# Optimization experiments

Measured on AMD Instinct MI355X. Metric: run time of the kernel, lower is better.

## Reference

```python
import jax, jax.numpy as jnp
import numpy as np

PS = 16
E = 512          # embed_dim
H = 8            # num_heads
EPS = 1e-5


def _ln(x, g, b):
    m = jnp.mean(x, axis=-1, keepdims=True)
    v = jnp.mean((x - m) ** 2, axis=-1, keepdims=True)
    return (x - m) * jax.lax.rsqrt(v + EPS) * g + b


def _mha(q_in, kv_in, in_w, in_b, out_w, out_b):
    # torch nn.MultiheadAttention: packed in_proj [3E, E], out_proj [E, E]
    Bq, Lq, _ = q_in.shape
    Lk = kv_in.shape[1]
    d = E // H
    wq, wk, wv = jnp.split(in_w, 3, axis=0)
    bq, bk, bv = jnp.split(in_b, 3, axis=0)
    q = (q_in @ wq.T + bq).reshape(Bq, Lq, H, d)
    k = (kv_in @ wk.T + bk).reshape(Bq, Lk, H, d)
    v = (kv_in @ wv.T + bv).reshape(Bq, Lk, H, d)
    scores = jnp.einsum('bqhd,bkhd->bhqk', q, k) / jnp.sqrt(jnp.float32(d))
    a = jax.nn.softmax(scores, axis=-1)
    o = jnp.einsum('bhqk,bkhd->bqhd', a, v).reshape(Bq, Lq, E)
    return o @ out_w.T + out_b


def setup_inputs() -> dict:
    key = jax.random.key(0)
    ks = jax.random.split(key, 24)
    s = 0.02
    D = 3 * PS * PS
    inp = {
        'neighbor_patches': jax.random.normal(ks[0], (8, 32, 32, 9, 3, PS, PS), jnp.float32),
        'w_pe': jax.random.normal(ks[1], (E, D), jnp.float32) * s,
        'b_pe': jnp.zeros((E,), jnp.float32),
        'pos_embed': jax.random.normal(ks[2], (1, 9, E), jnp.float32),
        'sa_in_w': jax.random.normal(ks[3], (3 * E, E), jnp.float32) * s,
        'sa_in_b': jnp.zeros((3 * E,), jnp.float32),
        'sa_out_w': jax.random.normal(ks[4], (E, E), jnp.float32) * s,
        'sa_out_b': jnp.zeros((E,), jnp.float32),
        'g1': jnp.ones((E,), jnp.float32), 'beta1': jnp.zeros((E,), jnp.float32),
        'ca_in_w': jax.random.normal(ks[5], (3 * E, E), jnp.float32) * s,
        'ca_in_b': jnp.zeros((3 * E,), jnp.float32),
        'ca_out_w': jax.random.normal(ks[6], (E, E), jnp.float32) * s,
        'ca_out_b': jnp.zeros((E,), jnp.float32),
        'g2': jnp.ones((E,), jnp.float32), 'beta2': jnp.zeros((E,), jnp.float32),
        'w1': jax.random.normal(ks[7], (4 * E, E), jnp.float32) * s,
        'b1': jnp.zeros((4 * E,), jnp.float32),
        'w2': jax.random.normal(ks[8], (E, 4 * E), jnp.float32) * s,
        'b2': jnp.zeros((E,), jnp.float32),
        'g3': jnp.ones((E,), jnp.float32), 'beta3': jnp.zeros((E,), jnp.float32),
    }
    return inp


def reference(neighbor_patches, w_pe, b_pe, pos_embed,
              sa_in_w, sa_in_b, sa_out_w, sa_out_b, g1, beta1,
              ca_in_w, ca_in_b, ca_out_w, ca_out_b, g2, beta2,
              w1, b1, w2, b2, g3, beta3):
    B, NH, NW, NN, C, ps, _ = neighbor_patches.shape
    x = neighbor_patches.reshape(B * NH * NW, NN, C * ps * ps)
    x = x @ w_pe.T + b_pe                       # [BN, 9, E]
    x = x + pos_embed
    attn = _mha(x, x, sa_in_w, sa_in_b, sa_out_w, sa_out_b)
    x = _ln(x + attn, g1, beta1)
    cq = x[:, 4:5, :]                            # center query [BN, 1, E]
    attn = _mha(cq, x, ca_in_w, ca_in_b, ca_out_w, ca_out_b)
    c = _ln(cq + attn, g2, beta2)
    ffn = jax.nn.gelu(c @ w1.T + b1, approximate=False) @ w2.T + b2
    out = _ln(c + ffn, g3, beta3)
    return out[:, 0, :].reshape(B, NH * NW, E)
```

## Files before the change

### kernel.cpp

```cpp
#include <hip/hip_runtime.h>


typedef unsigned short u16;
typedef u16   u16x8 __attribute__((ext_vector_type(8)));
typedef u16   u16x4 __attribute__((ext_vector_type(4)));
typedef __bf16 bf16x8 __attribute__((ext_vector_type(8)));
typedef __bf16 bf16x4 __attribute__((ext_vector_type(4)));
typedef float f32x4 __attribute__((ext_vector_type(4)));

static __device__ __forceinline__ u16 f2bf(float f) {
  union { float f; unsigned u; } v; v.f = f;
  unsigned r = v.u + 0x7FFFu + ((v.u >> 16) & 1u);
  return (u16)(r >> 16);
}
static __device__ __forceinline__ float bf2f(u16 u) {
  union { unsigned u; float f; } v; v.u = ((unsigned)u) << 16;
  return v.f;
}

static __device__ __forceinline__ void gld16(const void* g, void* l) {
  __builtin_amdgcn_global_load_lds(
      (__attribute__((address_space(1))) unsigned int*)(size_t)g,
      (__attribute__((address_space(3))) unsigned int*)(unsigned)(size_t)l,
      16, 0, 0);
}

static __device__ __forceinline__ int xcd_swz(int bid, int nwg) {
  int q = nwg >> 3, r = nwg & 7;
  int xcd = bid & 7, sub = bid >> 3;
  return (xcd < r ? xcd * (q + 1) : r * (q + 1) + (xcd - r) * q) + sub;
}

#define BAR   __builtin_amdgcn_s_barrier()
#define VM0   asm volatile("s_waitcnt vmcnt(0)" ::: "memory")
#define VM2   asm volatile("s_waitcnt vmcnt(2)" ::: "memory")
#define LGKM0 asm volatile("s_waitcnt lgkmcnt(0)" ::: "memory")

template<bool A_F32, bool HAS_POS, bool HAS_RES, bool HAS_GELU>
__global__ __launch_bounds__(256, 4) void gemm_k2(
    const void* Av, int lda,
    const u16* __restrict__ W,
    const float* __restrict__ bias,
    const float* __restrict__ pos,
    const u16* res, int res_stride,
    u16* out,
    int M, int N, int K, int nbx)
{
  __shared__ u16 As[2][4096];
  __shared__ u16 Bs[2][4096];

  const int t    = threadIdx.x;
  const int lane = t & 63, wv = t >> 6;
  const int swz  = xcd_swz(blockIdx.x, gridDim.x);
  const int bm   = (swz / nbx) * 128, bn = (swz % nbx) * 128;
  const int wr   = wv >> 1, wc = wv & 1;

  const int srow = lane >> 2;
  const int skk  = (((lane & 3) ^ ((lane >> 3) & 3)) << 3);
  const int lr = lane & 15;
  const int rg = (((lane >> 4) ^ ((lr >> 1) & 3)) << 3);

  f32x4 acc[4][4] = {};
  float4 areg[4];

  auto stage = [&](int buf, int kt) {
    const u16* A = (const u16*)Av;
    #pragma unroll
    for (int c = 0; c < 2; ++c) {
      int rr = (wv + 4 * c) * 16 + srow;
      gld16(A + (size_t)(bm + rr) * lda + kt * 32 + skk, &As[buf][(wv + 4 * c) * 512]);
      gld16(W + (size_t)(bn + rr) * K   + kt * 32 + skk, &Bs[buf][(wv + 4 * c) * 512]);
    }
  };
  auto stageB = [&](int buf, int kt) {
    #pragma unroll
    for (int c = 0; c < 2; ++c) {
      int rr = (wv + 4 * c) * 16 + srow;
      gld16(W + (size_t)(bn + rr) * K + kt * 32 + skk, &Bs[buf][(wv + 4 * c) * 512]);
    }
  };
  auto loadAf32 = [&](int kt) {
    const float* A = (const float*)Av;
    #pragma unroll
    for (int i = 0; i < 4; ++i) {
      int idx = i * 256 + t, r = idx >> 3, c4 = (idx & 7) * 4;
      areg[i] = *(const float4*)(A + (size_t)(bm + r) * lda + kt * 32 + c4);
    }
  };
  auto writeAf32 = [&](int buf) {
    #pragma unroll
    for (int i = 0; i < 4; ++i) {
      int idx = i * 256 + t, r = idx >> 3, c4 = (idx & 7) * 4;
      int g = (c4 >> 3) ^ ((r >> 1) & 3);
      int off = r * 32 + g * 8 + (c4 & 4);
      bf16x4 h;
      h.x = (__bf16)areg[i].x; h.y = (__bf16)areg[i].y;
      h.z = (__bf16)areg[i].z; h.w = (__bf16)areg[i].w;
      *(u16x4*)&As[buf][off] = *(u16x4*)&h;
    }
  };

  const int nkt = K >> 5;
  if constexpr (A_F32) {
    loadAf32(0); stageB(0, 0);
    VM2;  writeAf32(0);
    VM0; LGKM0; BAR;
  } else {
    stage(0, 0);
    VM0; BAR;
  }

  int cur = 0;
  for (int kt = 0; kt < nkt; ++kt) {
    const bool pf = (kt + 1 < nkt);
    if (pf) {
      if constexpr (A_F32) { loadAf32(kt + 1); stageB(cur ^ 1, kt + 1); }
      else                 { stage(cur ^ 1, kt + 1); }
    }

    bf16x8 a[4], b[4];
    #pragma unroll
    for (int m = 0; m < 4; ++m)
      a[m] = *(const bf16x8*)&As[cur][(wr * 64 + m * 16 + lr) * 32 + rg];
    #pragma unroll
    for (int n = 0; n < 4; ++n)
      b[n] = *(const bf16x8*)&Bs[cur][(wc * 64 + n * 16 + lr) * 32 + rg];
    #pragma unroll
    for (int m = 0; m < 4; ++m)
      #pragma unroll
      for (int n = 0; n < 4; ++n)
        acc[m][n] = __builtin_amdgcn_mfma_f32_16x16x32_bf16(a[m], b[n], acc[m][n], 0, 0, 0);

    if (pf) {
      if constexpr (A_F32) { VM2; writeAf32(cur ^ 1); VM0; LGKM0; }
      else                 { VM0; }
    }
    BAR;
    cur ^= 1;
  }

  const int lq = lane >> 4;
  #pragma unroll
  for (int m = 0; m < 4; ++m) {
    #pragma unroll
    for (int n = 0; n < 4; ++n) {
      int col = bn + wc * 64 + n * 16 + lr;
      float bv = bias[col];
      #pragma unroll
      for (int r = 0; r < 4; ++r) {
        int row = bm + wr * 64 + m * 16 + lq * 4 + r;
        float v = acc[m][n][r] + bv;
        if constexpr (HAS_POS) v += pos[(row % 9) * 512 + col];
        if constexpr (HAS_RES) v += bf2f(res[(size_t)row * res_stride + col]);
        if constexpr (HAS_GELU) v = 0.5f * v * (1.f + erff(v * 0.70710678118f));
        out[(size_t)row * N + col] = f2bf(v);
      }
    }
  }
}

__global__ __launch_bounds__(256) void ln_k(
    const u16* in,
    const float* __restrict__ g, const float* __restrict__ be,
    u16* out_bf, float* out_f32, int rows)
{
  int wv = threadIdx.x >> 6, lane = threadIdx.x & 63;
  int row = blockIdx.x * 4 + wv;
  if (row >= rows) return;
  const u16* p = in + (size_t)row * 512;
  u16x8 v = *(const u16x8*)&p[lane * 8];
  float x[8], s = 0.f, sq = 0.f;
  #pragma unroll
  for (int j = 0; j < 8; ++j) { x[j] = bf2f(v[j]); s += x[j]; sq += x[j] * x[j]; }
  #pragma unroll
  for (int o = 32; o > 0; o >>= 1) { s += __shfl_xor(s, o, 64); sq += __shfl_xor(sq, o, 64); }
  float mean = s * (1.f / 512.f);
  float var  = sq * (1.f / 512.f) - mean * mean;
  float rs   = rsqrtf(var + 1e-5f);
  float y[8];
  #pragma unroll
  for (int j = 0; j < 8; ++j) {
    int c = lane * 8 + j;
    y[j] = (x[j] - mean) * rs * g[c] + be[c];
  }
  if (out_bf) {
    u16x8 o8;
    #pragma unroll
    for (int j = 0; j < 8; ++j) o8[j] = f2bf(y[j]);
    *(u16x8*)&out_bf[(size_t)row * 512 + lane * 8] = o8;
  }
  if (out_f32) {
    #pragma unroll
    for (int j = 0; j < 8; ++j) out_f32[(size_t)row * 512 + lane * 8 + j] = y[j];
  }
}

__global__ __launch_bounds__(256) void sa_attn_k(const u16* __restrict__ qkv,
                                                 u16* __restrict__ out)
{
  __shared__ u16  s_qkv[9 * 1536];
  __shared__ float s_sc[8][81];
  const int s = blockIdx.x, t = threadIdx.x;
  const u16* src = qkv + (size_t)s * 9 * 1536;
  for (int i = t; i < (9 * 1536) / 8; i += 256)
    *(u16x8*)&s_qkv[i * 8] = *(const u16x8*)&src[i * 8];
  __syncthreads();

  const int h = t >> 5, sl = t & 31;
  for (int p = sl; p < 81; p += 32) {
    int qi = p / 9, ki = p % 9;
    const u16* qp = &s_qkv[qi * 1536 + h * 64];
    const u16* kp = &s_qkv[ki * 1536 + 512 + h * 64];
    float d = 0.f;
    #pragma unroll
    for (int e8 = 0; e8 < 8; ++e8) {
      u16x8 qv = *(const u16x8*)&qp[e8 * 8];
      u16x8 kv = *(const u16x8*)&kp[e8 * 8];
      #pragma unroll
      for (int j = 0; j < 8; ++j) d += bf2f(qv[j]) * bf2f(kv[j]);
    }
    s_sc[h][p] = d * 0.125f;
  }
  __syncthreads();

  if (t < 72) {
    int hh = t / 9, qi = t % 9;
    float* sc = &s_sc[hh][qi * 9];
    float mx = sc[0];
    #pragma unroll
    for (int i = 1; i < 9; ++i) mx = fmaxf(mx, sc[i]);
    float e[9], sum = 0.f;
    #pragma unroll
    for (int i = 0; i < 9; ++i) { e[i] = __expf(sc[i] - mx); sum += e[i]; }
    float inv = 1.f / sum;
    #pragma unroll
    for (int i = 0; i < 9; ++i) sc[i] = e[i] * inv;
  }
  __syncthreads();

  for (int gidx = sl; gidx < 72; gidx += 32) {
    int qi = gidx >> 3, dg = gidx & 7;
    float a[8] = {};
    #pragma unroll
    for (int ki = 0; ki < 9; ++ki) {
      float pr = s_sc[h][qi * 9 + ki];
      u16x8 vv = *(const u16x8*)&s_qkv[ki * 1536 + 1024 + h * 64 + dg * 8];
      #pragma unroll
      for (int j = 0; j < 8; ++j) a[j] += pr * bf2f(vv[j]);
    }
    u16x8 o8;
    #pragma unroll
    for (int j = 0; j < 8; ++j) o8[j] = f2bf(a[j]);
    *(u16x8*)&out[((size_t)s * 9 + qi) * 512 + h * 64 + dg * 8] = o8;
  }
}

__global__ __launch_bounds__(256) void ca_attn_k(const u16* __restrict__ q,
                                                 const u16* __restrict__ kv,
                                                 u16* __restrict__ out)
{
  __shared__ u16  s_q[512];
  __shared__ u16  s_kv[9 * 1024];
  __shared__ float s_sc[8][9];
  const int s = blockIdx.x, t = threadIdx.x;
  if (t < 64) *(u16x8*)&s_q[t * 8] = *(const u16x8*)&q[(size_t)s * 512 + t * 8];
  for (int i = t; i < (9 * 1024) / 8; i += 256)
    *(u16x8*)&s_kv[i * 8] = *(const u16x8*)&kv[(size_t)s * 9 * 1024 + i * 8];
  __syncthreads();

  if (t < 72) {
    int h = t / 9, ki = t % 9;
    const u16* qp = &s_q[h * 64];
    const u16* kp = &s_kv[ki * 1024 + h * 64];
    float d = 0.f;
    #pragma unroll
    for (int e8 = 0; e8 < 8; ++e8) {
      u16x8 qv = *(const u16x8*)&qp[e8 * 8];
      u16x8 kvv = *(const u16x8*)&kp[e8 * 8];
      #pragma unroll
      for (int j = 0; j < 8; ++j) d += bf2f(qv[j]) * bf2f(kvv[j]);
    }
    s_sc[h][ki] = d * 0.125f;
  }
  __syncthreads();

  if (t < 8) {
    float* sc = s_sc[t];
    float mx = sc[0];
    #pragma unroll
    for (int i = 1; i < 9; ++i) mx = fmaxf(mx, sc[i]);
    float e[9], sum = 0.f;
    #pragma unroll
    for (int i = 0; i < 9; ++i) { e[i] = __expf(sc[i] - mx); sum += e[i]; }
    float inv = 1.f / sum;
    #pragma unroll
    for (int i = 0; i < 9; ++i) sc[i] = e[i] * inv;
  }
  __syncthreads();

  if (t < 64) {
    int h = t >> 3, dg = t & 7;
    float a[8] = {};
    #pragma unroll
    for (int ki = 0; ki < 9; ++ki) {
      float pr = s_sc[h][ki];
      u16x8 vv = *(const u16x8*)&s_kv[ki * 1024 + 512 + h * 64 + dg * 8];
      #pragma unroll
      for (int j = 0; j < 8; ++j) a[j] += pr * bf2f(vv[j]);
    }
    u16x8 o8;
    #pragma unroll
    for (int j = 0; j < 8; ++j) o8[j] = f2bf(a[j]);
    *(u16x8*)&out[(size_t)s * 512 + h * 64 + dg * 8] = o8;
  }
}

__global__ __launch_bounds__(256) void wcvt_k(
    const float* s0, const float* s1, const float* s2, const float* s3,
    const float* s4, const float* s5, const float* s6, u16* dst)
{
  int b = blockIdx.x;
  const float* sp; long base, segStart;
  if      (b < 384)  { sp = s0; base = 0;       segStart = 0;    }
  else if (b < 1152) { sp = s1; base = 393216;  segStart = 384;  }
  else if (b < 1408) { sp = s2; base = 1179648; segStart = 1152; }
  else if (b < 2176) { sp = s3; base = 1441792; segStart = 1408; }
  else if (b < 2432) { sp = s4; base = 2228224; segStart = 2176; }
  else if (b < 3456) { sp = s5; base = 2490368; segStart = 2432; }
  else               { sp = s6; base = 3538944; segStart = 3456; }
  long loc = ((long)b - segStart) * 1024 + (long)threadIdx.x * 4;
  float4 f = *(const float4*)(sp + loc);
  u16x4 o; o.x = f2bf(f.x); o.y = f2bf(f.y); o.z = f2bf(f.z); o.w = f2bf(f.w);
  *(u16x4*)&dst[base + loc] = o;
}

extern "C" void kernel_launch(void* const* d_in, const int* in_sizes, int n_in,
                              void* d_out, int out_size, void* d_ws, size_t ws_size,
                              hipStream_t stream)
{
  const float* patches  = (const float*)d_in[0];
  const float* w_pe     = (const float*)d_in[1];
  const float* b_pe     = (const float*)d_in[2];
  const float* pos      = (const float*)d_in[3];
  const float* sa_in_w  = (const float*)d_in[4];
  const float* sa_in_b  = (const float*)d_in[5];
  const float* sa_out_w = (const float*)d_in[6];
  const float* sa_out_b = (const float*)d_in[7];
  const float* g1       = (const float*)d_in[8];
  const float* beta1    = (const float*)d_in[9];
  const float* ca_in_w  = (const float*)d_in[10];
  const float* ca_in_b  = (const float*)d_in[11];
  const float* ca_out_w = (const float*)d_in[12];
  const float* ca_out_b = (const float*)d_in[13];
  const float* g2       = (const float*)d_in[14];
  const float* beta2    = (const float*)d_in[15];
  const float* w1       = (const float*)d_in[16];
  const float* b1       = (const float*)d_in[17];
  const float* w2       = (const float*)d_in[18];
  const float* b2       = (const float*)d_in[19];
  const float* g3       = (const float*)d_in[20];
  const float* beta3    = (const float*)d_in[21];
  float* out = (float*)d_out;

  char* base = (char*)d_ws;
  u16* wbf        = (u16*)base;
  u16* w_pe_bf    = wbf;
  u16* sa_in_bf   = wbf + 393216;
  u16* sa_out_bf  = wbf + 1179648;
  u16* ca_in_bf   = wbf + 1441792;
  u16* ca_out_bf  = wbf + 2228224;
  u16* w1_bf      = wbf + 2490368;
  u16* w2_bf      = wbf + 3538944;
  u16* x_bf  = (u16*)(base + 9175040ull);
  u16* qkv   = (u16*)(base + 84672512ull);
  u16* sattn = (u16*)(base + 311164928ull);
  u16* q_bf  = (u16*)(base + 386662400ull);
  u16* cattn = (u16*)(base + 395051008ull);
  u16* csum  = (u16*)(base + 403439616ull);
  u16* h_bf  = (u16*)(base + 411828224ull);
  u16* osum  = (u16*)(base + 445382656ull);

  wcvt_k<<<4480, 256, 0, stream>>>(w_pe, sa_in_w, sa_out_w, ca_in_w,
                                   ca_out_w, w1, w2, wbf);

  gemm_k2<true, true, false, false><<<2304, 256, 0, stream>>>(
      patches, 768, w_pe_bf, b_pe, pos, nullptr, 0, x_bf, 73728, 512, 768, 4);
  gemm_k2<false, false, false, false><<<6912, 256, 0, stream>>>(
      x_bf, 512, sa_in_bf, sa_in_b, nullptr, nullptr, 0, qkv, 73728, 1536, 512, 12);
  sa_attn_k<<<8192, 256, 0, stream>>>(qkv, sattn);
  gemm_k2<false, false, true, false><<<2304, 256, 0, stream>>>(
      sattn, 512, sa_out_bf, sa_out_b, nullptr, x_bf, 512, x_bf, 73728, 512, 512, 4);
  ln_k<<<73728 / 4, 256, 0, stream>>>(x_bf, g1, beta1, x_bf, nullptr, 73728);
  gemm_k2<false, false, false, false><<<256, 256, 0, stream>>>(
      x_bf + 2048, 4608, ca_in_bf, ca_in_b, nullptr, nullptr, 0, q_bf, 8192, 512, 512, 4);
  gemm_k2<false, false, false, false><<<4608, 256, 0, stream>>>(
      x_bf, 512, ca_in_bf + 262144, ca_in_b + 512, nullptr, nullptr, 0, qkv, 73728, 1024, 512, 8);
  ca_attn_k<<<8192, 256, 0, stream>>>(q_bf, qkv, cattn);
  gemm_k2<false, false, true, false><<<256, 256, 0, stream>>>(
      cattn, 512, ca_out_bf, ca_out_b, nullptr, x_bf + 2048, 4608, csum, 8192, 512, 512, 4);
  ln_k<<<8192 / 4, 256, 0, stream>>>(csum, g2, beta2, csum, nullptr, 8192);
  gemm_k2<false, false, false, true><<<1024, 256, 0, stream>>>(
      csum, 512, w1_bf, b1, nullptr, nullptr, 0, h_bf, 8192, 2048, 512, 16);
  gemm_k2<false, false, true, false><<<256, 256, 0, stream>>>(
      h_bf, 2048, w2_bf, b2, nullptr, csum, 512, osum, 8192, 512, 2048, 4);
  ln_k<<<8192 / 4, 256, 0, stream>>>(osum, g3, beta3, nullptr, out, 8192);
}
```

Baseline: 782.7 us.

## Add 256x128-tile 512-thread GEMM kernel for large bf16 projections

```diff
diff --git a/kernel.cpp b/kernel.cpp
--- a/kernel.cpp
+++ b/kernel.cpp
@@ -35,6 +35,88 @@
 #define VM0   asm volatile("s_waitcnt vmcnt(0)" ::: "memory")
 #define VM2   asm volatile("s_waitcnt vmcnt(2)" ::: "memory")
 #define LGKM0 asm volatile("s_waitcnt lgkmcnt(0)" ::: "memory")
+
+template<bool HAS_RES, bool HAS_GELU>
+__global__ __launch_bounds__(512, 4) void gemm_t(
+    const u16* __restrict__ A, int lda,
+    const u16* __restrict__ W,
+    const float* __restrict__ bias,
+    const u16* res, int res_stride,
+    u16* out,
+    int M, int N, int K, int nbx)
+{
+  __shared__ u16 As[2][8192];
+  __shared__ u16 Bs[2][4096];
+
+  const int t    = threadIdx.x;
+  const int lane = t & 63, wv = t >> 6;
+  const int swz  = xcd_swz(blockIdx.x, gridDim.x);
+  const int bm   = (swz / nbx) * 256, bn = (swz % nbx) * 128;
+  const int wr   = wv >> 1, wc = wv & 1;
+
+  const int srow = lane >> 2;
+  const int skk  = (((lane & 3) ^ ((lane >> 3) & 3)) << 3);
+  const int lr = lane & 15;
+  const int rg = (((lane >> 4) ^ ((lr >> 1) & 3)) << 3);
+
+  f32x4 acc[4][4] = {};
+
+  auto stage = [&](int buf, int kt) {
+    #pragma unroll
+    for (int c = 0; c < 2; ++c) {
+      int rr = wv * 32 + c * 16 + srow;
+      gld16(A + (size_t)(bm + rr) * lda + kt * 32 + skk,
+            &As[buf][(wv * 2 + c) * 512]);
+    }
+    int rb = wv * 16 + srow;
+    gld16(W + (size_t)(bn + rb) * K + kt * 32 + skk, &Bs[buf][wv * 512]);
+  };
+
+  const int nkt = K >> 5;
+  stage(0, 0);
+  VM0; BAR;
+
+  int cur = 0;
+  for (int kt = 0; kt < nkt; ++kt) {
+    const bool pf = (kt + 1 < nkt);
+    if (pf) stage(cur ^ 1, kt + 1);
+
+    bf16x8 a[4], b[4];
+    #pragma unroll
+    for (int m = 0; m < 4; ++m)
+      a[m] = *(const bf16x8*)&As[cur][(wr * 64 + m * 16 + lr) * 32 + rg];
+    #pragma unroll
+    for (int n = 0; n < 4; ++n)
+      b[n] = *(const bf16x8*)&Bs[cur][(wc * 64 + n * 16 + lr) * 32 + rg];
+    #pragma unroll
+    for (int m = 0; m < 4; ++m)
+      #pragma unroll
+      for (int n = 0; n < 4; ++n)
+        acc[m][n] = __builtin_amdgcn_mfma_f32_16x16x32_bf16(a[m], b[n], acc[m][n], 0, 0, 0);
+
+    if (pf) VM0;
+    BAR;
+    cur ^= 1;
+  }
+
+  const int lq = lane >> 4;
+  #pragma unroll
+  for (int m = 0; m < 4; ++m) {
+    #pragma unroll
+    for (int n = 0; n < 4; ++n) {
+      int col = bn + wc * 64 + n * 16 + lr;
+      float bv = bias[col];
+      #pragma unroll
+      for (int r = 0; r < 4; ++r) {
+        int row = bm + wr * 64 + m * 16 + lq * 4 + r;
+        float v = acc[m][n][r] + bv;
+        if constexpr (HAS_RES) v += bf2f(res[(size_t)row * res_stride + col]);
+        if constexpr (HAS_GELU) v = 0.5f * v * (1.f + erff(v * 0.70710678118f));
+        out[(size_t)row * N + col] = f2bf(v);
+      }
+    }
+  }
+}
 
 template<bool A_F32, bool HAS_POS, bool HAS_RES, bool HAS_GELU>
 __global__ __launch_bounds__(256, 4) void gemm_k2(
@@ -385,22 +467,22 @@
 
   gemm_k2<true, true, false, false><<<2304, 256, 0, stream>>>(
       patches, 768, w_pe_bf, b_pe, pos, nullptr, 0, x_bf, 73728, 512, 768, 4);
-  gemm_k2<false, false, false, false><<<6912, 256, 0, stream>>>(
-      x_bf, 512, sa_in_bf, sa_in_b, nullptr, nullptr, 0, qkv, 73728, 1536, 512, 12);
+  gemm_t<false, false><<<3456, 512, 0, stream>>>(
+      x_bf, 512, sa_in_bf, sa_in_b, nullptr, 0, qkv, 73728, 1536, 512, 12);
   sa_attn_k<<<8192, 256, 0, stream>>>(qkv, sattn);
-  gemm_k2<false, false, true, false><<<2304, 256, 0, stream>>>(
-      sattn, 512, sa_out_bf, sa_out_b, nullptr, x_bf, 512, x_bf, 73728, 512, 512, 4);
+  gemm_t<true, false><<<1152, 512, 0, stream>>>(
+      sattn, 512, sa_out_bf, sa_out_b, x_bf, 512, x_bf, 73728, 512, 512, 4);
   ln_k<<<73728 / 4, 256, 0, stream>>>(x_bf, g1, beta1, x_bf, nullptr, 73728);
   gemm_k2<false, false, false, false><<<256, 256, 0, stream>>>(
       x_bf + 2048, 4608, ca_in_bf, ca_in_b, nullptr, nullptr, 0, q_bf, 8192, 512, 512, 4);
-  gemm_k2<false, false, false, false><<<4608, 256, 0, stream>>>(
-      x_bf, 512, ca_in_bf + 262144, ca_in_b + 512, nullptr, nullptr, 0, qkv, 73728, 1024, 512, 8);
+  gemm_t<false, false><<<2304, 512, 0, stream>>>(
+      x_bf, 512, ca_in_bf + 262144, ca_in_b + 512, nullptr, 0, qkv, 73728, 1024, 512, 8);
   ca_attn_k<<<8192, 256, 0, stream>>>(q_bf, qkv, cattn);
   gemm_k2<false, false, true, false><<<256, 256, 0, stream>>>(
       cattn, 512, ca_out_bf, ca_out_b, nullptr, x_bf + 2048, 4608, csum, 8192, 512, 512, 4);
   ln_k<<<8192 / 4, 256, 0, stream>>>(csum, g2, beta2, csum, nullptr, 8192);
-  gemm_k2<false, false, false, true><<<1024, 256, 0, stream>>>(
-      csum, 512, w1_bf, b1, nullptr, nullptr, 0, h_bf, 8192, 2048, 512, 16);
+  gemm_t<false, true><<<512, 512, 0, stream>>>(
+      csum, 512, w1_bf, b1, nullptr, 0, h_bf, 8192, 2048, 512, 16);
   gemm_k2<false, false, true, false><<<256, 256, 0, stream>>>(
       h_bf, 2048, w2_bf, b2, nullptr, csum, 512, osum, 8192, 512, 2048, 4);
   ln_k<<<8192 / 4, 256, 0, stream>>>(osum, g3, beta3, nullptr, out, 8192);
```

New measurement: 768.4 us. About the same (-1.8%).
